# Kernel optimization log

Measured on AMD Instinct MI355X. Metric: run time of the kernel, lower is better.

Reference implementation:

```python
import jax, jax.numpy as jnp
import numpy as np

GROUPS = 32
EPS = 1e-6


def group_norm(x, gamma, beta):
    B, C, H, W = x.shape
    xg = x.reshape(B, GROUPS, C // GROUPS, H, W)
    mu = xg.mean(axis=(2, 3, 4), keepdims=True)
    var = xg.var(axis=(2, 3, 4), keepdims=True)
    xn = ((xg - mu) / jnp.sqrt(var + EPS)).reshape(B, C, H, W)
    return xn * gamma[None, :, None, None] + beta[None, :, None, None]


def conv1x1(h, w, b):
    # 1x1 conv == channel matmul at every pixel
    return jnp.einsum('bchw,oc->bohw', h, w) + b[None, :, None, None]


def setup_inputs() -> dict:
    key = jax.random.key(0)
    ks = jax.random.split(key, 6)
    B, C, H, W = 2, 512, 64, 64
    s = 1.0 / np.sqrt(C)  # kaiming-ish scale for 1x1 conv weights
    return {
        'x': jax.random.normal(ks[0], (B, C, H, W), jnp.float32),
        'gn_gamma': jnp.ones((C,), jnp.float32),
        'gn_beta': jnp.zeros((C,), jnp.float32),
        'wq': jax.random.normal(ks[1], (C, C), jnp.float32) * s,
        'bq': jnp.zeros((C,), jnp.float32),
        'wk': jax.random.normal(ks[2], (C, C), jnp.float32) * s,
        'bk': jnp.zeros((C,), jnp.float32),
        'wv': jax.random.normal(ks[3], (C, C), jnp.float32) * s,
        'bv': jnp.zeros((C,), jnp.float32),
        'wp': jax.random.normal(ks[4], (C, C), jnp.float32) * s,
        'bp': jnp.zeros((C,), jnp.float32),
    }


def reference(x, gn_gamma, gn_beta, wq, bq, wk, bk, wv, bv, wp, bp):
    h = group_norm(x, gn_gamma, gn_beta)
    q = conv1x1(h, wq, bq)
    k = conv1x1(h, wk, bk)
    v = conv1x1(h, wv, bv)
    B, C, H, W = q.shape
    N = H * W
    qf = q.reshape(B, C, N)
    kf = k.reshape(B, C, N)
    vf = v.reshape(B, C, N)
    # scores[b,i,j] = sum_c q[b,c,i] * k[b,c,j], scaled by 1/sqrt(C)
    scores = jnp.einsum('bci,bcj->bij', qf, kf) * (C ** -0.5)
    attn = jax.nn.softmax(scores, axis=2)  # softmax over keys j
    # out[b,c,i] = sum_j v[b,c,j] * attn[b,i,j]
    out = jnp.einsum('bcj,bij->bci', vf, attn).reshape(B, C, H, W)
    out = conv1x1(out, wp, bp)
    return x + out
```

## Files before the change

kernel.cpp:

```cpp
#include <hip/hip_runtime.h>
#include <hip/hip_bf16.h>
#include <math.h>

#define CDIM 512
#define NPIX 4096
#define BATCH 2
#define NGROUP 32
#define CPG 16
#define EPSV 1e-6f

#define QT 64
#define KT 64
#define KSPLIT 2
#define KEYS_PER (NPIX / KSPLIT)
#define NKT (KEYS_PER / KT)

typedef __attribute__((ext_vector_type(4))) float f32x4;
typedef __attribute__((ext_vector_type(8))) short bf16x8;
typedef __attribute__((ext_vector_type(8))) unsigned short ushort8v;
typedef __attribute__((ext_vector_type(4))) unsigned short ushort4v;

__device__ inline unsigned short f2bf(float x) {
  __hip_bfloat16 h = __float2bfloat16(x);
  union { __hip_bfloat16 b; unsigned short u; } cv;
  cv.b = h;
  return cv.u;
}
__device__ inline float bf2f(unsigned short u) {
  union { __hip_bfloat16 b; unsigned short u; } cv;
  cv.u = u;
  return __bfloat162float(cv.b);
}

__device__ inline void gload_lds16(const void* g, void* l) {
  __builtin_amdgcn_global_load_lds((const __attribute__((address_space(1))) void*)g,
                                   (__attribute__((address_space(3))) void*)l, 16, 0, 0);
}

__global__ __launch_bounds__(1024)
void gn_kernel(const float* __restrict__ x, const float* __restrict__ gamma,
               const float* __restrict__ beta, float* __restrict__ h) {
  const int NE = CPG * NPIX;
  int b = blockIdx.x >> 5;
  int g = blockIdx.x & 31;
  size_t base = ((size_t)b * CDIM + (size_t)g * CPG) * NPIX;
  const float4* xv = (const float4*)(x + base);
  float4* hv = (float4*)(h + base);
  int t = threadIdx.x;
  float s = 0.f, ss = 0.f;
  for (int i = t; i < NE / 4; i += 1024) {
    float4 v = xv[i];
    s += (v.x + v.y) + (v.z + v.w);
    ss += v.x * v.x + v.y * v.y + v.z * v.z + v.w * v.w;
  }
#pragma unroll
  for (int off = 32; off >= 1; off >>= 1) {
    s += __shfl_down(s, off);
    ss += __shfl_down(ss, off);
  }
  __shared__ float redS[16], redQ[16];
  int wid = t >> 6;
  if ((t & 63) == 0) { redS[wid] = s; redQ[wid] = ss; }
  __syncthreads();
  __shared__ float s_mu, s_rs;
  if (t == 0) {
    float S = 0.f, Q = 0.f;
    for (int w = 0; w < 16; ++w) { S += redS[w]; Q += redQ[w]; }
    float mu = S / NE;
    float var = Q / NE - mu * mu;
    s_mu = mu;
    s_rs = rsqrtf(var + EPSV);
  }
  __syncthreads();
  float mu = s_mu, rs = s_rs;
  for (int i = t; i < NE / 4; i += 1024) {
    int c = g * CPG + (i >> 10);
    float ga = gamma[c] * rs;
    float be = beta[c] - mu * ga;
    float4 v = xv[i];
    v.x = v.x * ga + be;
    v.y = v.y * ga + be;
    v.z = v.z * ga + be;
    v.w = v.w * ga + be;
    hv[i] = v;
  }
}

#define BKc 16
#define WPAD 68

template <int MODE>
__global__ __launch_bounds__(256)
void conv1x1_kernel(const float* __restrict__ W, const float* __restrict__ bias,
                    const float* __restrict__ src, const float* __restrict__ resid,
                    float* __restrict__ dst, unsigned short* __restrict__ dsth,
                    unsigned short* __restrict__ dstl) {
  __shared__ __align__(16) float w_lds[BKc][WPAD];
  __shared__ __align__(16) float h_lds[BKc][64];
  __shared__ __align__(16) unsigned short t_lds[64][72];
  int t = threadIdx.x;
  int nBase = blockIdx.x * 64;
  int oBase = blockIdx.y * 64;
  int b = blockIdx.z;
  const float* srcb = src + (size_t)b * CDIM * NPIX;
  float acc[4][4] = {};
  int o0 = 4 * (t >> 4);
  int j0 = 4 * (t & 15);
  for (int c0 = 0; c0 < CDIM; c0 += BKc) {
    __syncthreads();
#pragma unroll
    for (int kk = 0; kk < 4; ++kk) {
      int idx = t + 256 * kk;
      int o_l = idx >> 4, c_l = idx & 15;
      w_lds[c_l][o_l] = W[(size_t)(oBase + o_l) * CDIM + c0 + c_l];
    }
#pragma unroll
    for (int kk = 0; kk < 4; ++kk) {
      int idx = t + 256 * kk;
      int c_l = idx >> 6, j = idx & 63;
      h_lds[c_l][j] = srcb[(size_t)(c0 + c_l) * NPIX + nBase + j];
    }
    __syncthreads();
#pragma unroll
    for (int kk = 0; kk < BKc; ++kk) {
      float4 a = *(const float4*)&w_lds[kk][o0];
      float4 bv = *(const float4*)&h_lds[kk][j0];
      float av[4] = {a.x, a.y, a.z, a.w};
      float bb[4] = {bv.x, bv.y, bv.z, bv.w};
#pragma unroll
      for (int r = 0; r < 4; ++r)
#pragma unroll
        for (int s2 = 0; s2 < 4; ++s2) acc[r][s2] += av[r] * bb[s2];
    }
  }
  if (MODE == 0) {
#pragma unroll
    for (int r = 0; r < 4; ++r) {
      int o = oBase + o0 + r;
      float bi = bias[o];
      size_t off = ((size_t)b * CDIM + o) * NPIX + nBase + j0;
      float4 out;
      out.x = acc[r][0] + bi;
      out.y = acc[r][1] + bi;
      out.z = acc[r][2] + bi;
      out.w = acc[r][3] + bi;
      float4 rv = *(const float4*)(resid + off);
      out.x += rv.x; out.y += rv.y; out.z += rv.z; out.w += rv.w;
      *(float4*)(dst + off) = out;
    }
  } else if (MODE == 2) {
#pragma unroll
    for (int r = 0; r < 4; ++r) {
      int o = oBase + o0 + r;
      float bi = bias[o];
      size_t off = ((size_t)b * CDIM + o) * NPIX + nBase + j0;
      ushort4v hv, lv;
#pragma unroll
      for (int s2 = 0; s2 < 4; ++s2) {
        float val = acc[r][s2] + bi;
        unsigned short hu = f2bf(val);
        hv[s2] = hu;
        lv[s2] = f2bf(val - bf2f(hu));
      }
      *(ushort4v*)(dsth + off) = hv;
      *(ushort4v*)(dstl + off) = lv;
    }
  } else {
    float biv[4];
#pragma unroll
    for (int r = 0; r < 4; ++r) biv[r] = bias[oBase + o0 + r];
#pragma unroll
    for (int phase = 0; phase < 2; ++phase) {
      __syncthreads();
#pragma unroll
      for (int r = 0; r < 4; ++r)
#pragma unroll
        for (int s2 = 0; s2 < 4; ++s2) {
          float val = acc[r][s2] + biv[r];
          unsigned short hu = f2bf(val);
          t_lds[j0 + s2][o0 + r] = phase == 0 ? hu : f2bf(val - bf2f(hu));
        }
      __syncthreads();
      unsigned short* dp = phase == 0 ? dsth : dstl;
      int row = t >> 2, seg = t & 3;
      size_t goff = ((size_t)b * NPIX + nBase + row) * CDIM + oBase + seg * 16;
#pragma unroll
      for (int e = 0; e < 2; ++e)
        *(ushort8v*)(dp + goff + 8 * e) = *(ushort8v*)&t_lds[row][seg * 16 + 8 * e];
    }
  }
}

__global__ __launch_bounds__(256, 1)
void attn_kernel(const unsigned short* __restrict__ qt_hi, const unsigned short* __restrict__ qt_lo,
                 const unsigned short* __restrict__ kt_hi, const unsigned short* __restrict__ kt_lo,
                 const unsigned short* __restrict__ v_hi, const unsigned short* __restrict__ v_lo,
                 float* __restrict__ opart, float* __restrict__ mlbuf) {
  __shared__ __align__(16) unsigned short ktile[2][64 * 64];
  __shared__ __align__(16) unsigned short plds[64 * 72];
  __shared__ float flds[64];

  int t = threadIdx.x;
  int lane = t & 63;
  int w = t >> 6;
  int qtile = blockIdx.x, b = blockIdx.y, ks = blockIdx.z;
  int qBase = qtile * QT;

  const unsigned short* qh = qt_hi + ((size_t)b * NPIX + qBase) * CDIM;
  const unsigned short* ql = qt_lo + ((size_t)b * NPIX + qBase) * CDIM;
  const unsigned short* kh = kt_hi + ((size_t)b * NPIX + ks * KEYS_PER) * CDIM;
  const unsigned short* kl = kt_lo + ((size_t)b * NPIX + ks * KEYS_PER) * CDIM;
  const unsigned short* vh = v_hi + (size_t)b * CDIM * NPIX + ks * KEYS_PER;
  const unsigned short* vl = v_lo + (size_t)b * CDIM * NPIX + ks * KEYS_PER;

  const unsigned short* qrow_h = qh + (size_t)(16 * w + (lane & 15)) * CDIM + 8 * (lane >> 4);
  const unsigned short* qrow_l = ql + (size_t)(16 * w + (lane & 15)) * CDIM + 8 * (lane >> 4);
  bf16x8 qfh[16];
#pragma unroll
  for (int cc = 0; cc < 16; ++cc) qfh[cc] = *(const bf16x8*)(qrow_h + 32 * cc);

  f32x4 Oacc[4][8];
#pragma unroll
  for (int rg = 0; rg < 4; ++rg)
#pragma unroll
    for (int cf = 0; cf < 8; ++cf) Oacc[rg][cf] = (f32x4){0.f, 0.f, 0.f, 0.f};
  float mrow[4], lrow[4];
#pragma unroll
  for (int r = 0; r < 4; ++r) { mrow[r] = -1e30f; lrow[r] = 0.f; }

  const float scale = 0.044194173824159216f;

  for (int kt = 0; kt < NKT; ++kt) {
    f32x4 Sacc[4];
#pragma unroll
    for (int f = 0; f < 4; ++f) Sacc[f] = (f32x4){0.f, 0.f, 0.f, 0.f};
    for (int ch = 0; ch < 8; ++ch) {
      __syncthreads();
#pragma unroll
      for (int j = 0; j < 4; ++j) {
        int idx = w * 4 + j;
        int buf = idx >> 3;
        int sub = idx & 7;
        const unsigned short* src = buf ? kl : kh;
        int key = sub * 8 + (lane >> 3);
        int cb = (lane & 7) ^ ((lane >> 3) & 7);
        gload_lds16(src + (size_t)(kt * KT + key) * CDIM + ch * 64 + cb * 8,
                    &ktile[buf][sub * 512]);
      }
      __syncthreads();
#pragma unroll
      for (int sc = 0; sc < 2; ++sc) {
        int cc = ch * 2 + sc;
        bf16x8 qflo = *(const bf16x8*)(qrow_l + 32 * cc);
        int cbl = sc * 4 + (lane >> 4);
#pragma unroll
        for (int f = 0; f < 4; ++f) {
          int key = 16 * f + (lane & 15);
          int swz = cbl ^ (key & 7);
          bf16x8 bh = *(const bf16x8*)&ktile[0][key * 64 + swz * 8];
          bf16x8 bl = *(const bf16x8*)&ktile[1][key * 64 + swz * 8];
          Sacc[f] = __builtin_amdgcn_mfma_f32_16x16x32_bf16(qfh[cc], bh, Sacc[f], 0, 0, 0);
          Sacc[f] = __builtin_amdgcn_mfma_f32_16x16x32_bf16(qflo, bh, Sacc[f], 0, 0, 0);
          Sacc[f] = __builtin_amdgcn_mfma_f32_16x16x32_bf16(qfh[cc], bl, Sacc[f], 0, 0, 0);
        }
      }
    }
    float fscale[4];
#pragma unroll
    for (int r = 0; r < 4; ++r) {
      float sv[4];
#pragma unroll
      for (int f = 0; f < 4; ++f) sv[f] = Sacc[f][r] * scale;
      float mx = fmaxf(fmaxf(sv[0], sv[1]), fmaxf(sv[2], sv[3]));
#pragma unroll
      for (int off = 1; off <= 8; off <<= 1) mx = fmaxf(mx, __shfl_xor(mx, off));
      float mn = fmaxf(mrow[r], mx);
      float rs = 0.f;
      int prow = 16 * w + 4 * (lane >> 4) + r;
#pragma unroll
      for (int f = 0; f < 4; ++f) {
        float p = __expf(sv[f] - mn);
        rs += p;
        plds[prow * 72 + 16 * f + (lane & 15)] = f2bf(p);
      }
#pragma unroll
      for (int off = 1; off <= 8; off <<= 1) rs += __shfl_xor(rs, off);
      fscale[r] = __expf(mrow[r] - mn);
      lrow[r] = lrow[r] * fscale[r] + rs;
      mrow[r] = mn;
      if ((lane & 15) == 0) flds[prow] = fscale[r];
    }
    __syncthreads();
#pragma unroll
    for (int rg = 0; rg < 4; ++rg) {
      float fr[4];
#pragma unroll
      for (int r = 0; r < 4; ++r) fr[r] = flds[16 * rg + 4 * (lane >> 4) + r];
#pragma unroll
      for (int cf = 0; cf < 8; ++cf)
#pragma unroll
        for (int r = 0; r < 4; ++r) Oacc[rg][cf][r] *= fr[r];
    }
#pragma unroll
    for (int kc = 0; kc < 2; ++kc) {
      bf16x8 ap[4];
#pragma unroll
      for (int rg = 0; rg < 4; ++rg)
        ap[rg] = *(const bf16x8*)&plds[(16 * rg + (lane & 15)) * 72 + 32 * kc + 8 * (lane >> 4)];
#pragma unroll
      for (int cf = 0; cf < 8; ++cf) {
        int chan = 128 * w + 16 * cf + (lane & 15);
        size_t vo = (size_t)chan * NPIX + kt * KT + 32 * kc + 8 * (lane >> 4);
        bf16x8 bvh = *(const bf16x8*)(vh + vo);
        bf16x8 bvl = *(const bf16x8*)(vl + vo);
#pragma unroll
        for (int rg = 0; rg < 4; ++rg) {
          Oacc[rg][cf] = __builtin_amdgcn_mfma_f32_16x16x32_bf16(ap[rg], bvh, Oacc[rg][cf], 0, 0, 0);
          Oacc[rg][cf] = __builtin_amdgcn_mfma_f32_16x16x32_bf16(ap[rg], bvl, Oacc[rg][cf], 0, 0, 0);
        }
      }
    }
  }
  size_t obase = ((size_t)b * KSPLIT + ks) * CDIM * (size_t)NPIX;
#pragma unroll
  for (int rg = 0; rg < 4; ++rg)
#pragma unroll
    for (int cf = 0; cf < 8; ++cf) {
      int chan = 128 * w + 16 * cf + (lane & 15);
#pragma unroll
      for (int r = 0; r < 4; ++r) {
        int row = 16 * rg + 4 * (lane >> 4) + r;
        opart[obase + (size_t)chan * NPIX + qBase + row] = Oacc[rg][cf][r];
      }
    }
  if ((lane & 15) == 0) {
    size_t mlb = ((size_t)b * KSPLIT + ks) * NPIX;
#pragma unroll
    for (int r = 0; r < 4; ++r) {
      int row = 16 * w + 4 * (lane >> 4) + r;
      mlbuf[(mlb + qBase + row) * 2 + 0] = mrow[r];
      mlbuf[(mlb + qBase + row) * 2 + 1] = lrow[r];
    }
  }
}

__global__ __launch_bounds__(256)
void combine_kernel(const float* __restrict__ opart, const float* __restrict__ mlbuf,
                    float* __restrict__ ao) {
  size_t idx = (size_t)blockIdx.x * 256 + threadIdx.x;
  size_t e = idx * 4;
  int i = (int)(e & (NPIX - 1));
  size_t bc = e >> 12;
  int b = (int)(bc >> 9);
  size_t o0 = ((size_t)b * KSPLIT + 0) * CDIM * (size_t)NPIX + (bc & 511) * (size_t)NPIX + i - ((size_t)b * CDIM * NPIX - (size_t)b * CDIM * NPIX);
  size_t c = bc & 511;
  size_t base0 = (((size_t)b * KSPLIT + 0) * CDIM + c) * NPIX + i;
  size_t base1 = (((size_t)b * KSPLIT + 1) * CDIM + c) * NPIX + i;
  float4 v0 = *(const float4*)(opart + base0);
  float4 v1 = *(const float4*)(opart + base1);
  float4 out;
  size_t ml0 = ((size_t)b * KSPLIT + 0) * NPIX;
  size_t ml1 = ((size_t)b * KSPLIT + 1) * NPIX;
  float o0v[4] = {v0.x, v0.y, v0.z, v0.w};
  float o1v[4] = {v1.x, v1.y, v1.z, v1.w};
  float res[4];
#pragma unroll
  for (int k = 0; k < 4; ++k) {
    float m0 = mlbuf[(ml0 + i + k) * 2 + 0], l0 = mlbuf[(ml0 + i + k) * 2 + 1];
    float m1 = mlbuf[(ml1 + i + k) * 2 + 0], l1 = mlbuf[(ml1 + i + k) * 2 + 1];
    float M = fmaxf(m0, m1);
    float w0 = __expf(m0 - M), w1 = __expf(m1 - M);
    res[k] = (w0 * o0v[k] + w1 * o1v[k]) / (w0 * l0 + w1 * l1);
  }
  out.x = res[0]; out.y = res[1]; out.z = res[2]; out.w = res[3];
  *(float4*)(ao + (bc * NPIX) + i) = out;
}

extern "C" void kernel_launch(void* const* d_in, const int* in_sizes, int n_in,
                              void* d_out, int out_size, void* d_ws, size_t ws_size,
                              hipStream_t stream) {
  const float* x     = (const float*)d_in[0];
  const float* gamma = (const float*)d_in[1];
  const float* beta  = (const float*)d_in[2];
  const float* wq    = (const float*)d_in[3];
  const float* bq    = (const float*)d_in[4];
  const float* wk    = (const float*)d_in[5];
  const float* bk    = (const float*)d_in[6];
  const float* wv    = (const float*)d_in[7];
  const float* bv    = (const float*)d_in[8];
  const float* wp    = (const float*)d_in[9];
  const float* bp    = (const float*)d_in[10];
  float* out = (float*)d_out;

  const size_t per = (size_t)BATCH * CDIM * NPIX;
  char* ws = (char*)d_ws;
  float* opart = (float*)ws;
  float* h = (float*)ws;
  unsigned short* qt_hi = (unsigned short*)(ws + 2 * per * 4);
  unsigned short* qt_lo = qt_hi + per;
  unsigned short* kt_hi = qt_lo + per;
  unsigned short* kt_lo = kt_hi + per;
  unsigned short* v_hi  = kt_lo + per;
  unsigned short* v_lo  = v_hi + per;
  float* ao = (float*)qt_hi;
  float* mlbuf = (float*)(ws + 2 * per * 4 + 6 * per * 2);

  gn_kernel<<<dim3(BATCH * NGROUP), dim3(1024), 0, stream>>>(x, gamma, beta, h);
  dim3 cgrid(NPIX / 64, CDIM / 64, BATCH);
  conv1x1_kernel<1><<<cgrid, 256, 0, stream>>>(wq, bq, h, nullptr, nullptr, qt_hi, qt_lo);
  conv1x1_kernel<1><<<cgrid, 256, 0, stream>>>(wk, bk, h, nullptr, nullptr, kt_hi, kt_lo);
  conv1x1_kernel<2><<<cgrid, 256, 0, stream>>>(wv, bv, h, nullptr, nullptr, v_hi, v_lo);
  attn_kernel<<<dim3(NPIX / QT, BATCH, KSPLIT), 256, 0, stream>>>(qt_hi, qt_lo, kt_hi, kt_lo,
                                                                  v_hi, v_lo, opart, mlbuf);
  combine_kernel<<<dim3((unsigned)(per / 4 / 256)), 256, 0, stream>>>(opart, mlbuf, ao);
  conv1x1_kernel<0><<<cgrid, 256, 0, stream>>>(wp, bp, ao, x, out, nullptr, nullptr);
}
```

Before: 808.3 us.

## Split attention keys four ways, double-buffer K tiles, and transpose partial outputs

```diff
diff --git a/kernel.cpp b/kernel.cpp
--- a/kernel.cpp
+++ b/kernel.cpp
@@ -11,9 +11,6 @@
 
 #define QT 64
 #define KT 64
-#define KSPLIT 2
-#define KEYS_PER (NPIX / KSPLIT)
-#define NKT (KEYS_PER / KT)
 
 typedef __attribute__((ext_vector_type(4))) float f32x4;
 typedef __attribute__((ext_vector_type(8))) short bf16x8;
@@ -21,9 +18,8 @@
 typedef __attribute__((ext_vector_type(4))) unsigned short ushort4v;
 
 __device__ inline unsigned short f2bf(float x) {
-  __hip_bfloat16 h = __float2bfloat16(x);
   union { __hip_bfloat16 b; unsigned short u; } cv;
-  cv.b = h;
+  cv.b = __float2bfloat16(x);
   return cv.u;
 }
 __device__ inline float bf2f(unsigned short u) {
@@ -191,19 +187,35 @@
   }
 }
 
-__global__ __launch_bounds__(256, 1)
+template <int KS>
+__global__ __launch_bounds__(256, 2)
 void attn_kernel(const unsigned short* __restrict__ qt_hi, const unsigned short* __restrict__ qt_lo,
                  const unsigned short* __restrict__ kt_hi, const unsigned short* __restrict__ kt_lo,
                  const unsigned short* __restrict__ v_hi, const unsigned short* __restrict__ v_lo,
                  float* __restrict__ opart, float* __restrict__ mlbuf) {
-  __shared__ __align__(16) unsigned short ktile[2][64 * 64];
+  const int KEYS_PER = NPIX / KS;
+  const int NKT = KEYS_PER / KT;
+  __shared__ __align__(16) unsigned short ktile[2][2][64 * 64];
   __shared__ __align__(16) unsigned short plds[64 * 72];
   __shared__ float flds[64];
 
   int t = threadIdx.x;
   int lane = t & 63;
+  int l15 = lane & 15;
+  int hh = lane >> 4;
   int w = t >> 6;
-  int qtile = blockIdx.x, b = blockIdx.y, ks = blockIdx.z;
+  int bid = blockIdx.x;
+  int qtile, b, ks;
+  if (KS == 4) {
+    int g = bid & 7;
+    b = g & 1;
+    ks = g >> 1;
+    qtile = bid >> 3;
+  } else {
+    qtile = bid & 63;
+    b = (bid >> 6) & 1;
+    ks = bid >> 7;
+  }
   int qBase = qtile * QT;
 
   const unsigned short* qh = qt_hi + ((size_t)b * NPIX + qBase) * CDIM;
@@ -213,11 +225,8 @@
   const unsigned short* vh = v_hi + (size_t)b * CDIM * NPIX + ks * KEYS_PER;
   const unsigned short* vl = v_lo + (size_t)b * CDIM * NPIX + ks * KEYS_PER;
 
-  const unsigned short* qrow_h = qh + (size_t)(16 * w + (lane & 15)) * CDIM + 8 * (lane >> 4);
-  const unsigned short* qrow_l = ql + (size_t)(16 * w + (lane & 15)) * CDIM + 8 * (lane >> 4);
-  bf16x8 qfh[16];
-#pragma unroll
-  for (int cc = 0; cc < 16; ++cc) qfh[cc] = *(const bf16x8*)(qrow_h + 32 * cc);
+  const unsigned short* qrow_h = qh + (size_t)(16 * w + l15) * CDIM + 8 * hh;
+  const unsigned short* qrow_l = ql + (size_t)(16 * w + l15) * CDIM + 8 * hh;
 
   f32x4 Oacc[4][8];
 #pragma unroll
@@ -230,42 +239,56 @@
 
   const float scale = 0.044194173824159216f;
 
+  auto issue = [&](int ch, int d, int ktof) {
+#pragma unroll
+    for (int j = 0; j < 4; ++j) {
+      int idx = w * 4 + j;
+      int hl = idx >> 3;
+      int sub = idx & 7;
+      const unsigned short* src = hl ? kl : kh;
+      int key = sub * 8 + (lane >> 3);
+      int cb = (lane & 7) ^ ((lane >> 3) & 7);
+      gload_lds16(src + (size_t)(ktof + key) * CDIM + ch * 64 + cb * 8,
+                  &ktile[d][hl][sub * 512]);
+    }
+  };
+
+  issue(0, 0, 0);
+
   for (int kt = 0; kt < NKT; ++kt) {
+    int ktof = kt * KT;
     f32x4 Sacc[4];
 #pragma unroll
     for (int f = 0; f < 4; ++f) Sacc[f] = (f32x4){0.f, 0.f, 0.f, 0.f};
     for (int ch = 0; ch < 8; ++ch) {
-      __syncthreads();
-#pragma unroll
-      for (int j = 0; j < 4; ++j) {
-        int idx = w * 4 + j;
-        int buf = idx >> 3;
-        int sub = idx & 7;
-        const unsigned short* src = buf ? kl : kh;
-        int key = sub * 8 + (lane >> 3);
-        int cb = (lane & 7) ^ ((lane >> 3) & 7);
-        gload_lds16(src + (size_t)(kt * KT + key) * CDIM + ch * 64 + cb * 8,
-                    &ktile[buf][sub * 512]);
-      }
-      __syncthreads();
+      int d = ch & 1;
+      if (ch < 7) {
+        issue(ch + 1, (ch + 1) & 1, ktof);
+        asm volatile("s_waitcnt vmcnt(4)" ::: "memory");
+      } else {
+        asm volatile("s_waitcnt vmcnt(0)" ::: "memory");
+      }
+      __builtin_amdgcn_s_barrier();
 #pragma unroll
       for (int sc = 0; sc < 2; ++sc) {
         int cc = ch * 2 + sc;
-        bf16x8 qflo = *(const bf16x8*)(qrow_l + 32 * cc);
-        int cbl = sc * 4 + (lane >> 4);
+        bf16x8 qfh_ = *(const bf16x8*)(qrow_h + 32 * cc);
+        bf16x8 qfl_ = *(const bf16x8*)(qrow_l + 32 * cc);
+        int cbl = sc * 4 + hh;
 #pragma unroll
         for (int f = 0; f < 4; ++f) {
-          int key = 16 * f + (lane & 15);
+          int key = 16 * f + l15;
           int swz = cbl ^ (key & 7);
-          bf16x8 bh = *(const bf16x8*)&ktile[0][key * 64 + swz * 8];
-          bf16x8 bl = *(const bf16x8*)&ktile[1][key * 64 + swz * 8];
-          Sacc[f] = __builtin_amdgcn_mfma_f32_16x16x32_bf16(qfh[cc], bh, Sacc[f], 0, 0, 0);
-          Sacc[f] = __builtin_amdgcn_mfma_f32_16x16x32_bf16(qflo, bh, Sacc[f], 0, 0, 0);
-          Sacc[f] = __builtin_amdgcn_mfma_f32_16x16x32_bf16(qfh[cc], bl, Sacc[f], 0, 0, 0);
+          bf16x8 bh = *(const bf16x8*)&ktile[d][0][key * 64 + swz * 8];
+          bf16x8 bl = *(const bf16x8*)&ktile[d][1][key * 64 + swz * 8];
+          Sacc[f] = __builtin_amdgcn_mfma_f32_16x16x32_bf16(qfh_, bh, Sacc[f], 0, 0, 0);
+          Sacc[f] = __builtin_amdgcn_mfma_f32_16x16x32_bf16(qfl_, bh, Sacc[f], 0, 0, 0);
+          Sacc[f] = __builtin_amdgcn_mfma_f32_16x16x32_bf16(qfh_, bl, Sacc[f], 0, 0, 0);
         }
       }
-    }
-    float fscale[4];
+      __builtin_amdgcn_s_barrier();
+    }
+    if (kt + 1 < NKT) issue(0, 0, ktof + KT);
 #pragma unroll
     for (int r = 0; r < 4; ++r) {
       float sv[4];
@@ -276,26 +299,27 @@
       for (int off = 1; off <= 8; off <<= 1) mx = fmaxf(mx, __shfl_xor(mx, off));
       float mn = fmaxf(mrow[r], mx);
       float rs = 0.f;
-      int prow = 16 * w + 4 * (lane >> 4) + r;
+      int prow = 16 * w + 4 * hh + r;
 #pragma unroll
       for (int f = 0; f < 4; ++f) {
         float p = __expf(sv[f] - mn);
         rs += p;
-        plds[prow * 72 + 16 * f + (lane & 15)] = f2bf(p);
+        plds[prow * 72 + 16 * f + l15] = f2bf(p);
       }
 #pragma unroll
       for (int off = 1; off <= 8; off <<= 1) rs += __shfl_xor(rs, off);
-      fscale[r] = __expf(mrow[r] - mn);
-      lrow[r] = lrow[r] * fscale[r] + rs;
+      float fs = __expf(mrow[r] - mn);
+      lrow[r] = lrow[r] * fs + rs;
       mrow[r] = mn;
-      if ((lane & 15) == 0) flds[prow] = fscale[r];
-    }
-    __syncthreads();
+      if (l15 == 0) flds[prow] = fs;
+    }
+    asm volatile("s_waitcnt lgkmcnt(0)" ::: "memory");
+    __builtin_amdgcn_s_barrier();
 #pragma unroll
     for (int rg = 0; rg < 4; ++rg) {
       float fr[4];
 #pragma unroll
-      for (int r = 0; r < 4; ++r) fr[r] = flds[16 * rg + 4 * (lane >> 4) + r];
+      for (int r = 0; r < 4; ++r) fr[r] = flds[16 * rg + 4 * hh + r];
 #pragma unroll
       for (int cf = 0; cf < 8; ++cf)
 #pragma unroll
@@ -306,11 +330,11 @@
       bf16x8 ap[4];
 #pragma unroll
       for (int rg = 0; rg < 4; ++rg)
-        ap[rg] = *(const bf16x8*)&plds[(16 * rg + (lane & 15)) * 72 + 32 * kc + 8 * (lane >> 4)];
+        ap[rg] = *(const bf16x8*)&plds[(16 * rg + l15) * 72 + 32 * kc + 8 * hh];
 #pragma unroll
       for (int cf = 0; cf < 8; ++cf) {
-        int chan = 128 * w + 16 * cf + (lane & 15);
-        size_t vo = (size_t)chan * NPIX + kt * KT + 32 * kc + 8 * (lane >> 4);
+        int chan = 128 * w + 16 * cf + l15;
+        size_t vo = (size_t)chan * NPIX + ktof + 32 * kc + 8 * hh;
         bf16x8 bvh = *(const bf16x8*)(vh + vo);
         bf16x8 bvl = *(const bf16x8*)(vl + vo);
 #pragma unroll
@@ -321,59 +345,79 @@
       }
     }
   }
-  size_t obase = ((size_t)b * KSPLIT + ks) * CDIM * (size_t)NPIX;
+  size_t obase = (size_t)(b * KS + ks) * NPIX * CDIM;
 #pragma unroll
   for (int rg = 0; rg < 4; ++rg)
 #pragma unroll
     for (int cf = 0; cf < 8; ++cf) {
-      int chan = 128 * w + 16 * cf + (lane & 15);
+      int chan = 128 * w + 16 * cf + l15;
 #pragma unroll
       for (int r = 0; r < 4; ++r) {
-        int row = 16 * rg + 4 * (lane >> 4) + r;
-        opart[obase + (size_t)chan * NPIX + qBase + row] = Oacc[rg][cf][r];
-      }
-    }
-  if ((lane & 15) == 0) {
-    size_t mlb = ((size_t)b * KSPLIT + ks) * NPIX;
+        int row = 16 * rg + 4 * hh + r;
+        opart[obase + (size_t)(qBase + row) * CDIM + chan] = Oacc[rg][cf][r];
+      }
+    }
+  if (l15 == 0) {
+    size_t mlb = (size_t)(b * KS + ks) * NPIX;
 #pragma unroll
     for (int r = 0; r < 4; ++r) {
-      int row = 16 * w + 4 * (lane >> 4) + r;
+      int row = 16 * w + 4 * hh + r;
       mlbuf[(mlb + qBase + row) * 2 + 0] = mrow[r];
       mlbuf[(mlb + qBase + row) * 2 + 1] = lrow[r];
     }
   }
 }
 
+template <int KS>
 __global__ __launch_bounds__(256)
 void combine_kernel(const float* __restrict__ opart, const float* __restrict__ mlbuf,
                     float* __restrict__ ao) {
-  size_t idx = (size_t)blockIdx.x * 256 + threadIdx.x;
-  size_t e = idx * 4;
-  int i = (int)(e & (NPIX - 1));
-  size_t bc = e >> 12;
-  int b = (int)(bc >> 9);
-  size_t o0 = ((size_t)b * KSPLIT + 0) * CDIM * (size_t)NPIX + (bc & 511) * (size_t)NPIX + i - ((size_t)b * CDIM * NPIX - (size_t)b * CDIM * NPIX);
-  size_t c = bc & 511;
-  size_t base0 = (((size_t)b * KSPLIT + 0) * CDIM + c) * NPIX + i;
-  size_t base1 = (((size_t)b * KSPLIT + 1) * CDIM + c) * NPIX + i;
-  float4 v0 = *(const float4*)(opart + base0);
-  float4 v1 = *(const float4*)(opart + base1);
-  float4 out;
-  size_t ml0 = ((size_t)b * KSPLIT + 0) * NPIX;
-  size_t ml1 = ((size_t)b * KSPLIT + 1) * NPIX;
-  float o0v[4] = {v0.x, v0.y, v0.z, v0.w};
-  float o1v[4] = {v1.x, v1.y, v1.z, v1.w};
-  float res[4];
-#pragma unroll
-  for (int k = 0; k < 4; ++k) {
-    float m0 = mlbuf[(ml0 + i + k) * 2 + 0], l0 = mlbuf[(ml0 + i + k) * 2 + 1];
-    float m1 = mlbuf[(ml1 + i + k) * 2 + 0], l1 = mlbuf[(ml1 + i + k) * 2 + 1];
-    float M = fmaxf(m0, m1);
-    float w0 = __expf(m0 - M), w1 = __expf(m1 - M);
-    res[k] = (w0 * o0v[k] + w1 * o1v[k]) / (w0 * l0 + w1 * l1);
-  }
-  out.x = res[0]; out.y = res[1]; out.z = res[2]; out.w = res[3];
-  *(float4*)(ao + (bc * NPIX) + i) = out;
+  __shared__ float tl[64][67];
+  __shared__ float wn[KS][64];
+  int t = threadIdx.x;
+  int r0 = blockIdx.x * 64, c0 = blockIdx.y * 64, b = blockIdx.z;
+  if (t < 64) {
+    int row = r0 + t;
+    float m[KS], l[KS], M = -1e30f;
+#pragma unroll
+    for (int ks = 0; ks < KS; ++ks) {
+      m[ks] = mlbuf[((size_t)(b * KS + ks) * NPIX + row) * 2 + 0];
+      l[ks] = mlbuf[((size_t)(b * KS + ks) * NPIX + row) * 2 + 1];
+      M = fmaxf(M, m[ks]);
+    }
+    float den = 0.f;
+#pragma unroll
+    for (int ks = 0; ks < KS; ++ks) den += __expf(m[ks] - M) * l[ks];
+    float rden = 1.f / den;
+#pragma unroll
+    for (int ks = 0; ks < KS; ++ks) wn[ks][t] = __expf(m[ks] - M) * rden;
+  }
+  __syncthreads();
+  int rr = t >> 4;
+  int cc = (t & 15) * 4;
+#pragma unroll
+  for (int p = 0; p < 4; ++p) {
+    int row = rr + 16 * p;
+    float ax = 0.f, ay = 0.f, az = 0.f, aw = 0.f;
+#pragma unroll
+    for (int ks = 0; ks < KS; ++ks) {
+      const float* src = opart + ((size_t)(b * KS + ks) * NPIX + r0 + row) * CDIM + c0 + cc;
+      float4 v = *(const float4*)src;
+      float wv = wn[ks][row];
+      ax += wv * v.x; ay += wv * v.y; az += wv * v.z; aw += wv * v.w;
+    }
+    tl[row][cc + 0] = ax; tl[row][cc + 1] = ay; tl[row][cc + 2] = az; tl[row][cc + 3] = aw;
+  }
+  __syncthreads();
+  int ch2 = t >> 4;
+  int rw = (t & 15) * 4;
+#pragma unroll
+  for (int p = 0; p < 4; ++p) {
+    int chn = ch2 + 16 * p;
+    float4 o;
+    o.x = tl[rw + 0][chn]; o.y = tl[rw + 1][chn]; o.z = tl[rw + 2][chn]; o.w = tl[rw + 3][chn];
+    *(float4*)(ao + ((size_t)b * CDIM + c0 + chn) * NPIX + r0 + rw) = o;
+  }
 }
 
 extern "C" void kernel_launch(void* const* d_in, const int* in_sizes, int n_in,
@@ -393,25 +437,35 @@
   float* out = (float*)d_out;
 
   const size_t per = (size_t)BATCH * CDIM * NPIX;
+  size_t need4 = 4 * per * 4 + 6 * per * 2 + (size_t)4 * BATCH * NPIX * 2 * 4;
+  const int KS = (ws_size >= need4) ? 4 : 2;
+
   char* ws = (char*)d_ws;
   float* opart = (float*)ws;
   float* h = (float*)ws;
-  unsigned short* qt_hi = (unsigned short*)(ws + 2 * per * 4);
+  unsigned short* qt_hi = (unsigned short*)(ws + (size_t)KS * per * 4);
   unsigned short* qt_lo = qt_hi + per;
   unsigned short* kt_hi = qt_lo + per;
   unsigned short* kt_lo = kt_hi + per;
   unsigned short* v_hi  = kt_lo + per;
   unsigned short* v_lo  = v_hi + per;
+  float* mlbuf = (float*)(ws + (size_t)KS * per * 4 + 6 * per * 2);
   float* ao = (float*)qt_hi;
-  float* mlbuf = (float*)(ws + 2 * per * 4 + 6 * per * 2);
 
   gn_kernel<<<dim3(BATCH * NGROUP), dim3(1024), 0, stream>>>(x, gamma, beta, h);
   dim3 cgrid(NPIX / 64, CDIM / 64, BATCH);
   conv1x1_kernel<1><<<cgrid, 256, 0, stream>>>(wq, bq, h, nullptr, nullptr, qt_hi, qt_lo);
   conv1x1_kernel<1><<<cgrid, 256, 0, stream>>>(wk, bk, h, nullptr, nullptr, kt_hi, kt_lo);
   conv1x1_kernel<2><<<cgrid, 256, 0, stream>>>(wv, bv, h, nullptr, nullptr, v_hi, v_lo);
-  attn_kernel<<<dim3(NPIX / QT, BATCH, KSPLIT), 256, 0, stream>>>(qt_hi, qt_lo, kt_hi, kt_lo,
-                                                                  v_hi, v_lo, opart, mlbuf);
-  combine_kernel<<<dim3((unsigned)(per / 4 / 256)), 256, 0, stream>>>(opart, mlbuf, ao);
+  dim3 mgrid(NPIX / 64, CDIM / 64, BATCH);
+  if (KS == 4) {
+    attn_kernel<4><<<dim3(64 * BATCH * 4), 256, 0, stream>>>(qt_hi, qt_lo, kt_hi, kt_lo,
+                                                             v_hi, v_lo, opart, mlbuf);
+    combine_kernel<4><<<mgrid, 256, 0, stream>>>(opart, mlbuf, ao);
+  } else {
+    attn_kernel<2><<<dim3(64 * BATCH * 2), 256, 0, stream>>>(qt_hi, qt_lo, kt_hi, kt_lo,
+                                                             v_hi, v_lo, opart, mlbuf);
+    combine_kernel<2><<<mgrid, 256, 0, stream>>>(opart, mlbuf, ao);
+  }
   conv1x1_kernel<0><<<cgrid, 256, 0, stream>>>(wp, bp, ao, x, out, nullptr, nullptr);
 }
```

Result: faster. 763.8 us (-5.5%).
